# Kernel tuning notes

Hardware: AMD Instinct MI355X
Metric: run time of the kernel (lower is better)

The kernel has to match this reference:

```python
import jax, jax.numpy as jnp
import numpy as np

D_MODEL = 1024
N_HEADS = 16
HEAD_DIM = D_MODEL // N_HEADS
NUM_SINK = 4
WINDOW = 512
B, S = 1, 4096


def _sink_visible(S):
    # visible[i, j] = (j <= i) & ((j < NUM_SINK) | (j >= i - WINDOW + 1))
    i = jnp.arange(S)[:, None]
    j = jnp.arange(S)[None, :]
    return (j <= i) & ((j < NUM_SINK) | (j >= i - WINDOW + 1))


def setup_inputs() -> dict:
    key = jax.random.key(0)
    kx, kq, kk, kv, ko = jax.random.split(key, 5)
    sc = 1.0 / np.sqrt(D_MODEL)
    return {
        "x": jax.random.normal(kx, (B, S, D_MODEL), dtype=jnp.float32),
        "Wq": jax.random.normal(kq, (D_MODEL, D_MODEL), dtype=jnp.float32) * sc,
        "Wk": jax.random.normal(kk, (D_MODEL, D_MODEL), dtype=jnp.float32) * sc,
        "Wv": jax.random.normal(kv, (D_MODEL, D_MODEL), dtype=jnp.float32) * sc,
        "Wo": jax.random.normal(ko, (D_MODEL, D_MODEL), dtype=jnp.float32) * sc,
    }


def reference(x, Wq, Wk, Wv, Wo):
    Bx, Sx, D = x.shape
    H, hd = N_HEADS, HEAD_DIM
    # nn.Linear (no bias): y = x @ W^T
    q = (x @ Wq.T).reshape(Bx, Sx, H, hd).transpose(0, 2, 1, 3)  # (B,H,S,hd)
    k = (x @ Wk.T).reshape(Bx, Sx, H, hd).transpose(0, 2, 1, 3)
    v = (x @ Wv.T).reshape(Bx, Sx, H, hd).transpose(0, 2, 1, 3)
    scale = 1.0 / np.sqrt(hd)
    scores = jnp.einsum("bhqd,bhkd->bhqk", q, k) * scale  # (B,H,S,S)
    visible = _sink_visible(Sx)  # (S,S) bool; every row has j=i visible
    scores = jnp.where(visible[None, None], scores, -jnp.inf)
    attn = jax.nn.softmax(scores, axis=-1)
    out = jnp.einsum("bhqk,bhkd->bhqd", attn, v)
    out = out.transpose(0, 2, 1, 3).reshape(Bx, Sx, D)
    return out @ Wo.T
```

## Files before the change

kernel.cpp:

```cpp
#include <hip/hip_runtime.h>
#include <stdint.h>

#define AS1 __attribute__((address_space(1)))
#define AS3 __attribute__((address_space(3)))

typedef short short8 __attribute__((ext_vector_type(8)));
typedef unsigned short ushort8 __attribute__((ext_vector_type(8)));
typedef __bf16 bf16x8 __attribute__((ext_vector_type(8)));
typedef float floatx4 __attribute__((ext_vector_type(4)));

__device__ __forceinline__ floatx4 mfma16(short8 a, short8 b, floatx4 c) {
  return __builtin_amdgcn_mfma_f32_16x16x32_bf16(
      __builtin_bit_cast(bf16x8, a), __builtin_bit_cast(bf16x8, b), c, 0, 0, 0);
}

__device__ __forceinline__ unsigned short f2bf(float f) {
  uint32_t u = __builtin_bit_cast(uint32_t, f);
  u = (u + 0x7FFFu + ((u >> 16) & 1u)) >> 16;
  return (unsigned short)u;
}

__device__ __forceinline__ uint32_t cvt_pk_bf16(float a, float b) {
  uint32_t d;
  asm("v_cvt_pk_bf16_f32 %0, %1, %2" : "=v"(d) : "v"(a), "v"(b));
  return d;
}

__global__ __launch_bounds__(256) void convert_pack(
    const float4* __restrict__ x, const float4* __restrict__ wq,
    const float4* __restrict__ wk, const float4* __restrict__ wv,
    const float4* __restrict__ wo, ushort4* __restrict__ xb,
    ushort4* __restrict__ wqkvb, ushort4* __restrict__ wob) {
  int i = blockIdx.x * 256 + threadIdx.x;
  const float4* src;
  ushort4* dst;
  if (i < (1 << 20)) {
    src = x + i;
    dst = xb + i;
  } else {
    int t = i - (1 << 20);
    int r = t >> 18;
    int j = t & ((1 << 18) - 1);
    src = (r == 0 ? wq : r == 1 ? wk : r == 2 ? wv : wo) + j;
    dst = (r < 3) ? (wqkvb + (r << 18) + j) : (wob + j);
  }
  float4 v = *src;
  ushort4 o;
  o.x = f2bf(v.x);
  o.y = f2bf(v.y);
  o.z = f2bf(v.z);
  o.w = f2bf(v.w);
  *dst = o;
}

template <typename OutT>
__global__ __launch_bounds__(256) void gemm_bt(const unsigned short* __restrict__ A,
                                               const unsigned short* __restrict__ Bm,
                                               OutT* __restrict__ C, int N, int K) {
  __shared__ unsigned short lds[2][16 * 512];
  const int tid = threadIdx.x;
  const int lane = tid & 63;
  const int w = tid >> 6;
  const int wr = w >> 1, wc = w & 1;

  const int lid = blockIdx.y * gridDim.x + blockIdx.x;
  const int xcd = lid & 7;
  const int wgid = xcd * 96 + (lid >> 3);
  const int s = wgid >> 5, w5 = wgid & 31;
  const int mt = (s & 3) * 8 + (w5 & 7);
  const int nt = (s >> 2) * 4 + (w5 >> 3);
  const int tm = mt * 128, tn = nt * 128;
  const int lrow = lane & 15;
  const int lk = (lane >> 4) * 8;

  floatx4 acc[4][4];
#pragma unroll
  for (int i = 0; i < 4; ++i)
#pragma unroll
    for (int j = 0; j < 4; ++j) acc[i][j] = floatx4{0.f, 0.f, 0.f, 0.f};

  auto stage = [&](int buf, int k0) {
#pragma unroll
    for (int c = w * 4; c < w * 4 + 4; ++c) {
      const unsigned short* g;
      if (c < 8) {
        g = A + (size_t)(tm + c * 16 + lrow) * K + (k0 + lk);
      } else {
        g = Bm + (size_t)(tn + (c - 8) * 16 + lrow) * K + (k0 + lk);
      }
      __builtin_amdgcn_global_load_lds((const AS1 uint32_t*)g,
                                       (AS3 uint32_t*)(&lds[buf][c * 512]), 16, 0, 0);
    }
  };

  stage(0, 0);
  __syncthreads();

  const int T = K >> 5;
  for (int t = 0; t < T; ++t) {
    if (t + 1 < T) stage((t + 1) & 1, (t + 1) << 5);
    const unsigned short* L = lds[t & 1];
    short8 af[4], bf[4];
#pragma unroll
    for (int i = 0; i < 4; ++i)
      af[i] = *(const short8*)&L[(wr * 4 + i) * 512 + lane * 8];
#pragma unroll
    for (int j = 0; j < 4; ++j)
      bf[j] = *(const short8*)&L[(8 + wc * 4 + j) * 512 + lane * 8];
#pragma unroll
    for (int i = 0; i < 4; ++i)
#pragma unroll
      for (int j = 0; j < 4; ++j) acc[i][j] = mfma16(af[i], bf[j], acc[i][j]);
    __syncthreads();
  }

  const int r0 = (lane >> 4) * 4;
#pragma unroll
  for (int i = 0; i < 4; ++i)
#pragma unroll
    for (int j = 0; j < 4; ++j)
#pragma unroll
      for (int r = 0; r < 4; ++r) {
        int row = tm + wr * 64 + i * 16 + r0 + r;
        int col = tn + wc * 64 + j * 16 + lrow;
        float v = acc[i][j][r];
        if constexpr (sizeof(OutT) == 2)
          C[(size_t)row * N + col] = f2bf(v);
        else
          C[(size_t)row * N + col] = v;
      }
}

__global__ __launch_bounds__(256) void gemm64(const unsigned short* __restrict__ A,
                                              const unsigned short* __restrict__ Bm,
                                              float* __restrict__ C, int N, int K) {
  __shared__ unsigned short lds[2][12 * 512];
  const int tid = threadIdx.x;
  const int lane = tid & 63;
  const int w = tid >> 6;
  const int wr = w >> 1, wc = w & 1;

  const int lid = blockIdx.y * gridDim.x + blockIdx.x;
  const int xcd = lid & 7;
  const int wgid = xcd * 64 + (lid >> 3);
  const int s = wgid >> 5, w5 = wgid & 31;
  const int mt = (s & 3) * 16 + (w5 & 15);
  const int nt = (s >> 2) * 2 + (w5 >> 4);
  const int tm = mt * 64, tn = nt * 128;
  const int lrow = lane & 15;
  const int lk = (lane >> 4) * 8;

  floatx4 acc[2][4];
#pragma unroll
  for (int i = 0; i < 2; ++i)
#pragma unroll
    for (int j = 0; j < 4; ++j) acc[i][j] = floatx4{0.f, 0.f, 0.f, 0.f};

  auto stage = [&](int buf, int k0) {
#pragma unroll
    for (int c = w * 3; c < w * 3 + 3; ++c) {
      const unsigned short* g;
      if (c < 4) {
        g = A + (size_t)(tm + c * 16 + lrow) * K + (k0 + lk);
      } else {
        g = Bm + (size_t)(tn + (c - 4) * 16 + lrow) * K + (k0 + lk);
      }
      __builtin_amdgcn_global_load_lds((const AS1 uint32_t*)g,
                                       (AS3 uint32_t*)(&lds[buf][c * 512]), 16, 0, 0);
    }
  };

  stage(0, 0);
  __syncthreads();

  const int T = K >> 5;
  for (int t = 0; t < T; ++t) {
    if (t + 1 < T) stage((t + 1) & 1, (t + 1) << 5);
    const unsigned short* L = lds[t & 1];
    short8 af[2], bf[4];
#pragma unroll
    for (int i = 0; i < 2; ++i)
      af[i] = *(const short8*)&L[(wr * 2 + i) * 512 + lane * 8];
#pragma unroll
    for (int j = 0; j < 4; ++j)
      bf[j] = *(const short8*)&L[(4 + wc * 4 + j) * 512 + lane * 8];
#pragma unroll
    for (int i = 0; i < 2; ++i)
#pragma unroll
      for (int j = 0; j < 4; ++j) acc[i][j] = mfma16(af[i], bf[j], acc[i][j]);
    __syncthreads();
  }

  const int r0 = (lane >> 4) * 4;
#pragma unroll
  for (int i = 0; i < 2; ++i)
#pragma unroll
    for (int j = 0; j < 4; ++j)
#pragma unroll
      for (int r = 0; r < 4; ++r) {
        int row = tm + (wr * 2 + i) * 16 + r0 + r;
        int col = tn + (wc * 4 + j) * 16 + lrow;
        C[(size_t)row * N + col] = acc[i][j][r];
      }
}

__global__ __launch_bounds__(256) void attn_kernel(const unsigned short* __restrict__ qkv,
                                                   unsigned short* __restrict__ aout) {
  __shared__ unsigned short Klds[2][16 * 512];
  __shared__ unsigned short VT[64 * 136];
  __shared__ unsigned short PT[4][16 * 136];

  const int tid = threadIdx.x;
  const int lane = tid & 63;
  const int w = tid >> 6;
  const int lrow = lane & 15;
  const int lkg = lane >> 4;

  const int i = blockIdx.x;
  const int half = i >> 8;
  const int j = (i >> 3) & 31;
  const int h = 2 * (i & 7) + half;
  const int qb = half ? (31 - j) : j;
  const int q0 = qb * 128;

  short8 qf[2][2];
#pragma unroll
  for (int qt = 0; qt < 2; ++qt)
#pragma unroll
    for (int ks = 0; ks < 2; ++ks)
      qf[qt][ks] = *(const short8*)&qkv[(size_t)(q0 + qt * 64 + w * 16 + lrow) * 3072 +
                                        h * 64 + ks * 32 + lkg * 8];

  float m_i[2], l_i[2];
  floatx4 o[4][2];
#pragma unroll
  for (int qt = 0; qt < 2; ++qt) {
    m_i[qt] = -1e30f;
    l_i[qt] = 0.f;
#pragma unroll
    for (int nt = 0; nt < 4; ++nt) o[nt][qt] = floatx4{0.f, 0.f, 0.f, 0.f};
  }

  const float scale2 = 0.125f * 1.44269504088896f;

  if (w < 2) {
    const unsigned short* g = &qkv[(size_t)lrow * 3072 + 1024 + h * 64 + w * 32 + lkg * 8];
    __builtin_amdgcn_global_load_lds((const AS1 uint32_t*)g,
                                     (AS3 uint32_t*)(&Klds[0][w * 512]), 16, 0, 0);
  }
  {
    if (lane < 16) {
      const unsigned short* g0 = &qkv[(size_t)(2 * lane) * 3072 + 2048 + h * 64 + w * 16];
      ushort8 a0 = *(const ushort8*)g0;
      ushort8 a1 = *(const ushort8*)(g0 + 8);
      ushort8 b0 = *(const ushort8*)(g0 + 3072);
      ushort8 b1 = *(const ushort8*)(g0 + 3080);
      uint32_t* vt = (uint32_t*)VT;
#pragma unroll
      for (int dd = 0; dd < 8; ++dd) {
        vt[(w * 16 + dd) * 68 + lane] = (uint32_t)a0[dd] | ((uint32_t)b0[dd] << 16);
        vt[(w * 16 + 8 + dd) * 68 + lane] = (uint32_t)a1[dd] | ((uint32_t)b1[dd] << 16);
      }
    }
  }
  const int kb0 = (q0 - 511 < 16) ? 16 : (q0 - 511);
#pragma unroll
  for (int c = 0; c < 4; ++c) {
    int ch = w * 4 + c;
    int kt = ch >> 1, ks = ch & 1;
    const unsigned short* g =
        &qkv[(size_t)(kb0 + kt * 16 + lrow) * 3072 + 1024 + h * 64 + ks * 32 + lkg * 8];
    __builtin_amdgcn_global_load_lds((const AS1 uint32_t*)g,
                                     (AS3 uint32_t*)(&Klds[1][ch * 512]), 16, 0, 0);
  }
  ushort8 va0, va1, vb0, vb1;
  {
    const unsigned short* g0 = &qkv[(size_t)(kb0 + 2 * lane) * 3072 + 2048 + h * 64 + w * 16];
    va0 = *(const ushort8*)g0;
    va1 = *(const ushort8*)(g0 + 8);
    vb0 = *(const ushort8*)(g0 + 3072);
    vb1 = *(const ushort8*)(g0 + 3080);
  }
  __syncthreads();

#pragma unroll
  for (int qt = 0; qt < 2; ++qt) {
    const int qq = q0 + qt * 64 + w * 16 + lrow;
    floatx4 s0 = floatx4{0.f, 0.f, 0.f, 0.f};
#pragma unroll
    for (int ks = 0; ks < 2; ++ks) {
      short8 kf = *(const short8*)&Klds[0][ks * 512 + lane * 8];
      s0 = mfma16(kf, qf[qt][ks], s0);
    }
    float mx = -1e30f;
    float sv[4];
#pragma unroll
    for (int r = 0; r < 4; ++r) {
      int key = lkg * 4 + r;
      bool vis = (key <= qq) && ((key < 4) || (key >= qq - 511));
      sv[r] = vis ? s0[r] * scale2 : -1e30f;
      mx = fmaxf(mx, sv[r]);
    }
    mx = fmaxf(mx, __shfl_xor(mx, 16));
    mx = fmaxf(mx, __shfl_xor(mx, 32));
    m_i[qt] = mx;
    float p0 = exp2f(sv[0] - mx), p1 = exp2f(sv[1] - mx);
    float p2 = exp2f(sv[2] - mx), p3 = exp2f(sv[3] - mx);
    float ps = (p0 + p1) + (p2 + p3);
    *(uint2*)&PT[w][lrow * 136 + lkg * 4] = uint2{cvt_pk_bf16(p0, p1), cvt_pk_bf16(p2, p3)};
    *(uint2*)&PT[w][lrow * 136 + 16 + lkg * 4] = uint2{0u, 0u};
    ps += __shfl_xor(ps, 16);
    ps += __shfl_xor(ps, 32);
    l_i[qt] = ps;
    short8 pf = *(const short8*)&PT[w][lrow * 136 + lkg * 8];
#pragma unroll
    for (int nt = 0; nt < 4; ++nt) {
      short8 vf = *(const short8*)&VT[(nt * 16 + lrow) * 136 + lkg * 8];
      o[nt][qt] = mfma16(vf, pf, o[nt][qt]);
    }
  }

  int nbuf = 1;
  for (int kb = kb0; kb < q0 + 128; kb += 128) {
    const bool hasnext = (kb + 128 < q0 + 128);
    __syncthreads();
    {
      uint32_t* vt = (uint32_t*)VT;
#pragma unroll
      for (int dd = 0; dd < 8; ++dd) {
        vt[(w * 16 + dd) * 68 + lane] = (uint32_t)va0[dd] | ((uint32_t)vb0[dd] << 16);
        vt[(w * 16 + 8 + dd) * 68 + lane] = (uint32_t)va1[dd] | ((uint32_t)vb1[dd] << 16);
      }
    }
    __syncthreads();

    if (hasnext) {
      const int kn = kb + 128;
#pragma unroll
      for (int c = 0; c < 4; ++c) {
        int ch = w * 4 + c;
        int kt = ch >> 1, ks = ch & 1;
        const unsigned short* g =
            &qkv[(size_t)(kn + kt * 16 + lrow) * 3072 + 1024 + h * 64 + ks * 32 + lkg * 8];
        __builtin_amdgcn_global_load_lds((const AS1 uint32_t*)g,
                                         (AS3 uint32_t*)(&Klds[1 - nbuf][ch * 512]), 16, 0, 0);
      }
      const unsigned short* g0 = &qkv[(size_t)(kn + 2 * lane) * 3072 + 2048 + h * 64 + w * 16];
      va0 = *(const ushort8*)g0;
      va1 = *(const ushort8*)(g0 + 8);
      vb0 = *(const ushort8*)(g0 + 3072);
      vb1 = *(const ushort8*)(g0 + 3080);
    }

#pragma unroll
    for (int qt = 0; qt < 2; ++qt) {
      const int qaT = q0 + qt * 64 + w * 16;
      const int qq = qaT + lrow;
      floatx4 s[8];
#pragma unroll
      for (int ct = 0; ct < 8; ++ct) {
        s[ct] = floatx4{0.f, 0.f, 0.f, 0.f};
#pragma unroll
        for (int ks = 0; ks < 2; ++ks) {
          short8 kf = *(const short8*)&Klds[nbuf][(ct * 2 + ks) * 512 + lane * 8];
          s[ct] = mfma16(kf, qf[qt][ks], s[ct]);
        }
      }
      const bool full = (kb + 127 <= qaT) && (kb >= qaT + 15 - 511);
      float mx = -1e30f;
#pragma unroll
      for (int ct = 0; ct < 8; ++ct)
#pragma unroll
        for (int r = 0; r < 4; ++r) {
          float val = s[ct][r] * scale2;
          if (!full) {
            int key = kb + ct * 16 + lkg * 4 + r;
            bool vis = (key <= qq) && (key >= qq - 511);
            val = vis ? val : -1e30f;
          }
          s[ct][r] = val;
          mx = fmaxf(mx, val);
        }
      mx = fmaxf(mx, __shfl_xor(mx, 16));
      mx = fmaxf(mx, __shfl_xor(mx, 32));
      float nm = fmaxf(m_i[qt], mx);
      float alpha = exp2f(m_i[qt] - nm);
      m_i[qt] = nm;

      float ps = 0.f;
#pragma unroll
      for (int ct = 0; ct < 8; ++ct) {
        float p0 = exp2f(s[ct][0] - nm), p1 = exp2f(s[ct][1] - nm);
        float p2 = exp2f(s[ct][2] - nm), p3 = exp2f(s[ct][3] - nm);
        ps += (p0 + p1) + (p2 + p3);
        *(uint2*)&PT[w][lrow * 136 + ct * 16 + lkg * 4] =
            uint2{cvt_pk_bf16(p0, p1), cvt_pk_bf16(p2, p3)};
      }
      ps += __shfl_xor(ps, 16);
      ps += __shfl_xor(ps, 32);
      l_i[qt] = l_i[qt] * alpha + ps;

#pragma unroll
      for (int nt = 0; nt < 4; ++nt)
#pragma unroll
        for (int r = 0; r < 4; ++r) o[nt][qt][r] *= alpha;

#pragma unroll
      for (int kk = 0; kk < 4; ++kk) {
        short8 pf = *(const short8*)&PT[w][lrow * 136 + kk * 32 + lkg * 8];
#pragma unroll
        for (int nt = 0; nt < 4; ++nt) {
          short8 vf = *(const short8*)&VT[(nt * 16 + lrow) * 136 + kk * 32 + lkg * 8];
          o[nt][qt] = mfma16(vf, pf, o[nt][qt]);
        }
      }
    }
    nbuf ^= 1;
  }

#pragma unroll
  for (int qt = 0; qt < 2; ++qt) {
    const int qq = q0 + qt * 64 + w * 16 + lrow;
    const float inv = 1.0f / l_i[qt];
#pragma unroll
    for (int nt = 0; nt < 4; ++nt) {
      floatx4 ov = o[nt][qt];
      uint32_t lo = cvt_pk_bf16(ov[0] * inv, ov[1] * inv);
      uint32_t hi = cvt_pk_bf16(ov[2] * inv, ov[3] * inv);
      *(uint2*)&aout[(size_t)qq * 1024 + h * 64 + nt * 16 + lkg * 4] = uint2{lo, hi};
    }
  }
}

extern "C" void kernel_launch(void* const* d_in, const int* in_sizes, int n_in,
                              void* d_out, int out_size, void* d_ws, size_t ws_size,
                              hipStream_t stream) {
  const float* x = (const float*)d_in[0];
  const float* wq = (const float*)d_in[1];
  const float* wk = (const float*)d_in[2];
  const float* wv = (const float*)d_in[3];
  const float* wo = (const float*)d_in[4];

  char* ws = (char*)d_ws;
  unsigned short* Xb = (unsigned short*)(ws);
  unsigned short* Wqkv = (unsigned short*)(ws + (8u << 20));
  unsigned short* Wob = (unsigned short*)(ws + (14u << 20));
  unsigned short* QKV = (unsigned short*)(ws + (16u << 20));
  unsigned short* AO = (unsigned short*)(ws + (40u << 20));

  convert_pack<<<8192, 256, 0, stream>>>((const float4*)x, (const float4*)wq,
                                         (const float4*)wk, (const float4*)wv,
                                         (const float4*)wo, (ushort4*)Xb,
                                         (ushort4*)Wqkv, (ushort4*)Wob);
  gemm_bt<unsigned short><<<dim3(32, 24), 256, 0, stream>>>(Xb, Wqkv, QKV, 3072, 1024);
  attn_kernel<<<512, 256, 0, stream>>>(QKV, AO);
  gemm64<<<dim3(64, 8), 256, 0, stream>>>(AO, Wob, (float*)d_out, 1024, 1024);
}
```

Baseline: 195.1 us.

## Triple-buffer GEMM LDS staging with one barrier per K-step

Both projection GEMM kernels move from double to triple LDS buffering. Loads are issued two K-steps ahead, and each step waits with a partial vmcnt and a single s_barrier instead of two __syncthreads. This aims to hide more global-load latency and halve barrier overhead per iteration. It costs more LDS per block, which may reduce occupancy, and it relies on hand-counted vmcnt values matching the number of outstanding loads.

```diff
diff --git a/kernel.cpp b/kernel.cpp
--- a/kernel.cpp
+++ b/kernel.cpp
@@ -57,7 +57,7 @@
 __global__ __launch_bounds__(256) void gemm_bt(const unsigned short* __restrict__ A,
                                                const unsigned short* __restrict__ Bm,
                                                OutT* __restrict__ C, int N, int K) {
-  __shared__ unsigned short lds[2][16 * 512];
+  __shared__ unsigned short lds[3][16 * 512];
   const int tid = threadIdx.x;
   const int lane = tid & 63;
   const int w = tid >> 6;
@@ -79,7 +79,7 @@
 #pragma unroll
     for (int j = 0; j < 4; ++j) acc[i][j] = floatx4{0.f, 0.f, 0.f, 0.f};
 
-  auto stage = [&](int buf, int k0) {
+  auto stage = [&](unsigned short* buf, int k0) {
 #pragma unroll
     for (int c = w * 4; c < w * 4 + 4; ++c) {
       const unsigned short* g;
@@ -89,17 +89,11 @@
         g = Bm + (size_t)(tn + (c - 8) * 16 + lrow) * K + (k0 + lk);
       }
       __builtin_amdgcn_global_load_lds((const AS1 uint32_t*)g,
-                                       (AS3 uint32_t*)(&lds[buf][c * 512]), 16, 0, 0);
+                                       (AS3 uint32_t*)(buf + c * 512), 16, 0, 0);
     }
   };
 
-  stage(0, 0);
-  __syncthreads();
-
-  const int T = K >> 5;
-  for (int t = 0; t < T; ++t) {
-    if (t + 1 < T) stage((t + 1) & 1, (t + 1) << 5);
-    const unsigned short* L = lds[t & 1];
+  auto compute = [&](const unsigned short* L) {
     short8 af[4], bf[4];
 #pragma unroll
     for (int i = 0; i < 4; ++i)
@@ -111,8 +105,30 @@
     for (int i = 0; i < 4; ++i)
 #pragma unroll
       for (int j = 0; j < 4; ++j) acc[i][j] = mfma16(af[i], bf[j], acc[i][j]);
-    __syncthreads();
-  }
+  };
+
+  stage(lds[0], 0);
+  stage(lds[1], 32);
+
+  const int T = K >> 5;
+  int bt = 0;
+  for (int t = 0; t < T - 1; ++t) {
+    asm volatile("s_waitcnt vmcnt(4)" ::: "memory");
+    __builtin_amdgcn_sched_barrier(0);
+    __builtin_amdgcn_s_barrier();
+    __builtin_amdgcn_sched_barrier(0);
+    if (t + 2 < T) {
+      int b2 = (bt + 2 >= 3) ? bt - 1 : bt + 2;
+      stage(lds[b2], (t + 2) << 5);
+    }
+    compute(lds[bt]);
+    bt = (bt + 1 == 3) ? 0 : bt + 1;
+  }
+  asm volatile("s_waitcnt vmcnt(0)" ::: "memory");
+  __builtin_amdgcn_sched_barrier(0);
+  __builtin_amdgcn_s_barrier();
+  __builtin_amdgcn_sched_barrier(0);
+  compute(lds[bt]);
 
   const int r0 = (lane >> 4) * 4;
 #pragma unroll
@@ -134,7 +150,7 @@
 __global__ __launch_bounds__(256) void gemm64(const unsigned short* __restrict__ A,
                                               const unsigned short* __restrict__ Bm,
                                               float* __restrict__ C, int N, int K) {
-  __shared__ unsigned short lds[2][12 * 512];
+  __shared__ unsigned short lds[3][12 * 512];
   const int tid = threadIdx.x;
   const int lane = tid & 63;
   const int w = tid >> 6;
@@ -156,7 +172,7 @@
 #pragma unroll
     for (int j = 0; j < 4; ++j) acc[i][j] = floatx4{0.f, 0.f, 0.f, 0.f};
 
-  auto stage = [&](int buf, int k0) {
+  auto stage = [&](unsigned short* buf, int k0) {
 #pragma unroll
     for (int c = w * 3; c < w * 3 + 3; ++c) {
       const unsigned short* g;
@@ -166,17 +182,11 @@
         g = Bm + (size_t)(tn + (c - 4) * 16 + lrow) * K + (k0 + lk);
       }
       __builtin_amdgcn_global_load_lds((const AS1 uint32_t*)g,
-                                       (AS3 uint32_t*)(&lds[buf][c * 512]), 16, 0, 0);
+                                       (AS3 uint32_t*)(buf + c * 512), 16, 0, 0);
     }
   };
 
-  stage(0, 0);
-  __syncthreads();
-
-  const int T = K >> 5;
-  for (int t = 0; t < T; ++t) {
-    if (t + 1 < T) stage((t + 1) & 1, (t + 1) << 5);
-    const unsigned short* L = lds[t & 1];
+  auto compute = [&](const unsigned short* L) {
     short8 af[2], bf[4];
 #pragma unroll
     for (int i = 0; i < 2; ++i)
@@ -188,8 +198,30 @@
     for (int i = 0; i < 2; ++i)
 #pragma unroll
       for (int j = 0; j < 4; ++j) acc[i][j] = mfma16(af[i], bf[j], acc[i][j]);
-    __syncthreads();
-  }
+  };
+
+  stage(lds[0], 0);
+  stage(lds[1], 32);
+
+  const int T = K >> 5;
+  int bt = 0;
+  for (int t = 0; t < T - 1; ++t) {
+    asm volatile("s_waitcnt vmcnt(3)" ::: "memory");
+    __builtin_amdgcn_sched_barrier(0);
+    __builtin_amdgcn_s_barrier();
+    __builtin_amdgcn_sched_barrier(0);
+    if (t + 2 < T) {
+      int b2 = (bt + 2 >= 3) ? bt - 1 : bt + 2;
+      stage(lds[b2], (t + 2) << 5);
+    }
+    compute(lds[bt]);
+    bt = (bt + 1 == 3) ? 0 : bt + 1;
+  }
+  asm volatile("s_waitcnt vmcnt(0)" ::: "memory");
+  __builtin_amdgcn_sched_barrier(0);
+  __builtin_amdgcn_s_barrier();
+  __builtin_amdgcn_sched_barrier(0);
+  compute(lds[bt]);
 
   const int r0 = (lane >> 4) * 4;
 #pragma unroll
```

Result: no change. 193.4 us (-0.9%).
